# Kernel optimization log

Hardware: AMD Instinct MI355X
Metric: run time of the kernel (lower is better)

## Reference

```python
import jax, jax.numpy as jnp
import numpy as np

B, S, D = 2, 2048, 1024
H, DK, DV = 16, 64, 64
DFF = 4096
EPS_RMS = 1e-6


def setup_inputs() -> dict:
    key = jax.random.key(0)
    ks = jax.random.split(key, 10)
    sc = 0.02
    return {
        "x": jax.random.normal(ks[0], (B, S, D), jnp.float32),
        "w_q": jax.random.normal(ks[1], (D, H * DK), jnp.float32) * sc,
        "w_k": jax.random.normal(ks[2], (D, H * DK), jnp.float32) * sc,
        "w_v": jax.random.normal(ks[3], (D, H * DV), jnp.float32) * sc,
        "w_o": jax.random.normal(ks[4], (H * DV, D), jnp.float32) * sc,
        "w_gate": jax.random.normal(ks[5], (D, DFF), jnp.float32) * sc,
        "w_up": jax.random.normal(ks[6], (D, DFF), jnp.float32) * sc,
        "w_down": jax.random.normal(ks[7], (DFF, D), jnp.float32) * sc,
        "g1": jnp.ones((D,), jnp.float32),
        "g2": jnp.ones((D,), jnp.float32),
    }


def _rmsnorm(x, g):
    var = jnp.mean(jnp.square(x), axis=-1, keepdims=True)
    return x * jax.lax.rsqrt(var + EPS_RMS) * g


def _stable_softmax(s):
    # Faithful to source: exp(x) / (sum exp(x) + 1e-9); fully-masked rows -> 0.
    e = jnp.exp(s)
    return e / (jnp.sum(e, axis=-1, keepdims=True) + 1e-9)


def reference(x, w_q, w_k, w_v, w_o, w_gate, w_up, w_down, g1, g2):
    b, s, d = x.shape
    h = _rmsnorm(x, g1)
    q = (h @ w_q).reshape(b, s, H, DK).transpose(0, 2, 1, 3)  # [B,H,S,DK]
    k = (h @ w_k).reshape(b, s, H, DK).transpose(0, 2, 1, 3)
    v = (h @ w_v).reshape(b, s, H, DV).transpose(0, 2, 1, 3)
    scores = jnp.einsum("bhqd,bhkd->bhqk", q, k) / jnp.sqrt(jnp.asarray(DK, x.dtype))
    # triu with diagonal=0: self and future positions are masked
    mask = jnp.triu(jnp.ones((s, s), bool))
    scores = jnp.where(mask, -jnp.inf, scores)
    attn = _stable_softmax(scores)  # [B,H,S,S]
    av = jnp.einsum("bhqk,bhkd->bhqd", attn, v)
    av = av.transpose(0, 2, 1, 3).reshape(b, s, H * DV)
    x = x + av @ w_o  # residual 1
    h2 = _rmsnorm(x, g2)
    hidden = jax.nn.silu(h2 @ w_gate) * (h2 @ w_up)
    return x + hidden @ w_down  # residual 2
```

## Files before the change

kernel.cpp:

```cpp
#include <hip/hip_runtime.h>
#include <cstdint>
#include <cstddef>

typedef unsigned short u16;
typedef unsigned char u8;
typedef unsigned int u32;
typedef __bf16 bf16x8 __attribute__((ext_vector_type(8)));
typedef float floatx4 __attribute__((ext_vector_type(4)));
typedef float floatx16 __attribute__((ext_vector_type(16)));
typedef int i32x8 __attribute__((ext_vector_type(8)));

#define B_ 2
#define S_ 2048
#define D_ 1024
#define H_ 16
#define DFF_ 4096
#define BS_ 4096

__device__ __forceinline__ u16 f2bf(float f) {
  u32 u = __builtin_bit_cast(u32, f);
  u += 0x7fffu + ((u >> 16) & 1u);
  return (u16)(u >> 16);
}
__device__ __forceinline__ float bf2f(u16 h) {
  u32 u = ((u32)h) << 16;
  return __builtin_bit_cast(float, u);
}

__device__ __forceinline__ u32 cvtpk_bf16(float lo, float hi) {
  u32 r;
  asm("v_cvt_pk_bf16_f32 %0, %1, %2" : "=v"(r) : "v"(lo), "v"(hi));
  return r;
}

__device__ __forceinline__ float fexp2(float x) {
  float r;
  asm("v_exp_f32 %0, %1" : "=v"(r) : "v"(x));
  return r;
}

__device__ __forceinline__ u32 f2e4m3(float f) {
  u32 u = __builtin_bit_cast(u32, f);
  const u32 s = (u >> 24) & 0x80u;
  const u32 au = u & 0x7fffffffu;
  if (au < 0x3c800000u) return s;
  if (au > 0x43e00000u) return s | 0x7eu;
  const u32 lsb = (au >> 20) & 1u;
  const u32 r = au + 0x0007ffffu + lsb;
  const u32 e = (r >> 23) & 0xffu;
  const u32 m = (r >> 20) & 7u;
  return s | (((e - 120u) & 0xfu) << 3) | m;
}

__device__ __forceinline__ void gl_lds16(const void* g, void* l) {
  __builtin_amdgcn_global_load_lds(
      (const __attribute__((address_space(1))) void*)g,
      (__attribute__((address_space(3))) void*)l, 16, 0, 0);
}

__device__ __forceinline__ void xcd_swz(int GX, int GY, int& bx, int& by) {
  int flat = by * GX + bx;
  const int q = (GX * GY) >> 3;
  flat = (flat & 7) * q + (flat >> 3);
  bx = flat % GX;
  by = flat / GX;
}

#define WAITB(N) asm volatile("s_waitcnt vmcnt(" #N ")\n\ts_barrier" ::: "memory")

__global__ void prep_weights(const float* __restrict__ wq, const float* __restrict__ wk,
                             const float* __restrict__ wv, const float* __restrict__ wo,
                             const float* __restrict__ wg, const float* __restrict__ wu,
                             const float* __restrict__ wd,
                             u16* __restrict__ wqkv_t, u16* __restrict__ wo_t,
                             u8* __restrict__ wguf8, u16* __restrict__ wdn_t) {
  __shared__ float tile[32][33];
  const int id = blockIdx.x;
  const float* src;
  u16* dst = nullptr;
  int R, C, bx, by, mode;
  if (id < 3072) {
    const int which = id >> 10, lo = id & 1023;
    src = which == 0 ? wq : (which == 1 ? wk : wv);
    dst = wqkv_t + which * 1024 * 1024;
    R = 1024; C = 1024; bx = lo & 31; by = lo >> 5; mode = 0;
  } else if (id < 4096) {
    const int lo = id - 3072;
    src = wo; dst = wo_t; R = 1024; C = 1024; bx = lo & 31; by = lo >> 5; mode = 0;
  } else if (id < 8192) {
    const int lo = id - 4096;
    src = wg; R = 1024; C = 4096; bx = lo & 127; by = lo >> 7; mode = 1;
  } else if (id < 12288) {
    const int lo = id - 8192;
    src = wu; R = 1024; C = 4096; bx = lo & 127; by = lo >> 7; mode = 2;
  } else {
    const int lo = id - 12288;
    src = wd; dst = wdn_t; R = 4096; C = 1024; bx = lo & 31; by = lo >> 5; mode = 0;
  }
  const int tx = threadIdx.x, ty = threadIdx.y;
  const int c0 = bx * 32, r0 = by * 32;
#pragma unroll
  for (int i = 0; i < 4; i++)
    tile[ty + i * 8][tx] = src[(size_t)(r0 + ty + i * 8) * C + c0 + tx];
  __syncthreads();
  const int sx = ty * 32 + tx;
  const int oci = sx >> 3, cg = (sx & 7) * 4;
  const int oc = c0 + oci;
  const float v0 = tile[cg][oci], v1 = tile[cg + 1][oci];
  const float v2 = tile[cg + 2][oci], v3 = tile[cg + 3][oci];
  if (mode == 0) {
    uint2 o;
    o.x = (u32)f2bf(v0) | ((u32)f2bf(v1) << 16);
    o.y = (u32)f2bf(v2) | ((u32)f2bf(v3) << 16);
    *(uint2*)(dst + (size_t)oc * R + r0 + cg) = o;
  } else {
    const int orow = (oc >> 5) * 64 + (oc & 31) + (mode == 2 ? 32 : 0);
    const u32 p = f2e4m3(v0 * 64.f) | (f2e4m3(v1 * 64.f) << 8) |
                  (f2e4m3(v2 * 64.f) << 16) | (f2e4m3(v3 * 64.f) << 24);
    *(u32*)(wguf8 + (size_t)orow * 1024 + r0 + cg) = p;
  }
}

template <int F8>
__global__ __launch_bounds__(256) void rmsnorm_kernel(const float* __restrict__ x,
                                                      const float* __restrict__ g,
                                                      void* __restrict__ out) {
  const int row = blockIdx.x, t = threadIdx.x;
  const float4 v = ((const float4*)(x + (size_t)row * 1024))[t];
  float ss = v.x * v.x + v.y * v.y + v.z * v.z + v.w * v.w;
#pragma unroll
  for (int off = 32; off > 0; off >>= 1) ss += __shfl_xor(ss, off);
  __shared__ float red[4];
  if ((t & 63) == 0) red[t >> 6] = ss;
  __syncthreads();
  ss = red[0] + red[1] + red[2] + red[3];
  const float inv = rsqrtf(ss * (1.0f / 1024.0f) + 1e-6f);
  const float4 gv = ((const float4*)g)[t];
  const float y0 = v.x * inv * gv.x, y1 = v.y * inv * gv.y;
  const float y2 = v.z * inv * gv.z, y3 = v.w * inv * gv.w;
  if (F8) {
    const u32 p = f2e4m3(y0) | (f2e4m3(y1) << 8) | (f2e4m3(y2) << 16) | (f2e4m3(y3) << 24);
    ((u32*)out)[(size_t)row * 256 + t] = p;
  } else {
    uint2 o;
    o.x = (u32)f2bf(y0) | ((u32)f2bf(y1) << 16);
    o.y = (u32)f2bf(y2) | ((u32)f2bf(y3) << 16);
    ((uint2*)out)[(size_t)row * 256 + t] = o;
  }
}

template <int BN>
__device__ __forceinline__ void bt_step(const u16* Asb, const u16* Bsb,
                                        floatx16 (&acc)[2][BN / 64],
                                        int wm, int wn, int c31, int khalf) {
  constexpr int NTI = BN / 64;
#pragma unroll
  for (int ks = 0; ks < 4; ks++) {
    bf16x8 af[2], bfr[NTI];
#pragma unroll
    for (int mi = 0; mi < 2; mi++) {
      const int row = wm * 64 + mi * 32 + c31;
      const int e = (ks * 2 + khalf) ^ (row & 7);
      af[mi] = *(const bf16x8*)(Asb + row * 64 + e * 8);
    }
#pragma unroll
    for (int ni = 0; ni < NTI; ni++) {
      const int row = wn * (BN / 2) + ni * 32 + c31;
      const int e = (ks * 2 + khalf) ^ (row & 7);
      bfr[ni] = *(const bf16x8*)(Bsb + row * 64 + e * 8);
    }
    __builtin_amdgcn_s_setprio(1);
#pragma unroll
    for (int mi = 0; mi < 2; mi++)
#pragma unroll
      for (int ni = 0; ni < NTI; ni++)
        acc[mi][ni] = __builtin_amdgcn_mfma_f32_32x32x16_bf16(af[mi], bfr[ni],
                                                              acc[mi][ni], 0, 0, 0);
    __builtin_amdgcn_s_setprio(0);
  }
}

template <int SPW>
__device__ __forceinline__ void bt_issue(const u16* (&gsrc)[SPW], u16* const (&ld0)[SPW],
                                         int bufofs) {
#pragma unroll
  for (int i = 0; i < SPW; i++) gl_lds16(gsrc[i], ld0[i] + bufofs);
#pragma unroll
  for (int i = 0; i < SPW; i++) gsrc[i] += 64;
}

template <int BN, int EPI>
__global__ __launch_bounds__(256) void gemm_bt(const u16* __restrict__ A,
                                               const u16* __restrict__ Bt,
                                               void* __restrict__ Cout,
                                               const float* __restrict__ res,
                                               u16* __restrict__ vTout,
                                               int M, int N, int K) {
  constexpr int NTI = BN / 64;
  constexpr int ASZ = 128 * 64;
  constexpr int BSZ = BN * 64;
  constexpr int STRIDE = ASZ + BSZ;
  __shared__ u16 SMEM[3 * STRIDE];
  constexpr int NSEG = 16 + BN / 8;
  constexpr int SPW = NSEG / 4;
  static_assert(SPW == 6, "vmcnt literal assumes 6 loads/wave/tile");
  const int t = threadIdx.x, w = t >> 6, l = t & 63;

  int bx = (int)blockIdx.x, by = (int)blockIdx.y;
  xcd_swz((int)gridDim.x, (int)gridDim.y, bx, by);
  const int m0 = by * 128, n0 = bx * BN;
  const int wm = w >> 1, wn = w & 1;
  const int c31 = l & 31, khalf = l >> 5;

  const u16* gsrc[SPW];
  u16* ld0[SPW];
  {
    const int rl = l >> 3, ch = (l & 7) ^ rl;
#pragma unroll
    for (int i = 0; i < SPW; i++) {
      const int s = w * SPW + i;
      if (s < 16) {
        gsrc[i] = A + (size_t)(m0 + s * 8 + rl) * K + ch * 8;
        ld0[i] = SMEM + s * 512;
      } else {
        gsrc[i] = Bt + (size_t)(n0 + (s - 16) * 8 + rl) * K + ch * 8;
        ld0[i] = SMEM + ASZ + (s - 16) * 512;
      }
    }
  }

  floatx16 acc[2][NTI] = {};

#define BT_STEP(CB) bt_step<BN>(SMEM + (CB)*STRIDE, SMEM + (CB)*STRIDE + ASZ, \
                                acc, wm, wn, c31, khalf)

  bt_issue<SPW>(gsrc, ld0, 0 * STRIDE);
  bt_issue<SPW>(gsrc, ld0, 1 * STRIDE);
  const int NT = K >> 6;
  for (int rep = 0; rep < (NT - 4) / 3; rep++) {
    WAITB(6); bt_issue<SPW>(gsrc, ld0, 2 * STRIDE); BT_STEP(0);
    WAITB(6); bt_issue<SPW>(gsrc, ld0, 0 * STRIDE); BT_STEP(1);
    WAITB(6); bt_issue<SPW>(gsrc, ld0, 1 * STRIDE); BT_STEP(2);
  }
  WAITB(6); bt_issue<SPW>(gsrc, ld0, 2 * STRIDE); BT_STEP(0);
  WAITB(6); bt_issue<SPW>(gsrc, ld0, 0 * STRIDE); BT_STEP(1);
  WAITB(6); BT_STEP(2);
  WAITB(0); BT_STEP(0);
#undef BT_STEP

  if constexpr (EPI == 3) {
    if (n0 >= 2048) {
#pragma unroll
      for (int mi = 0; mi < 2; mi++)
#pragma unroll
        for (int ni = 0; ni < NTI; ni++) {
          const int col = n0 + wn * (BN / 2) + ni * 32 + c31 - 2048;
          const int hh = col >> 6, dv = col & 63;
          const int rbase = m0 + wm * 64 + mi * 32 + 4 * khalf;
          const int bb = rbase >> 11;
          u16* vp = vTout + (size_t)((bb * 16 + hh) * 64 + dv) * 2048 + (rbase & 2047);
#pragma unroll
          for (int rg = 0; rg < 4; rg++) {
            uint2 pk;
            pk.x = (u32)f2bf(acc[mi][ni][rg * 4 + 0]) |
                   ((u32)f2bf(acc[mi][ni][rg * 4 + 1]) << 16);
            pk.y = (u32)f2bf(acc[mi][ni][rg * 4 + 2]) |
                   ((u32)f2bf(acc[mi][ni][rg * 4 + 3]) << 16);
            *(uint2*)(vp + rg * 8) = pk;
          }
        }
      return;
    }
  }
#pragma unroll
  for (int mi = 0; mi < 2; mi++)
#pragma unroll
    for (int ni = 0; ni < NTI; ni++) {
      const int col = n0 + wn * (BN / 2) + ni * 32 + c31;
#pragma unroll
      for (int reg = 0; reg < 16; reg++) {
        const int row = m0 + wm * 64 + mi * 32 + (reg & 3) + 8 * (reg >> 2) + 4 * khalf;
        const size_t idx = (size_t)row * N + col;
        if (EPI == 1) ((float*)Cout)[idx] = acc[mi][ni][reg] + res[idx];
        else          ((u16*)Cout)[idx] = f2bf(acc[mi][ni][reg]);
      }
    }
}

__device__ __forceinline__ void f8_step(const u8* Asb, const u8* Bsb,
                                        floatx16 (&acc)[2][2],
                                        int wm, int wn, int c31, int hf) {
  i32x8 af[2], bf[2];
#pragma unroll
  for (int mi = 0; mi < 2; mi++) {
    const int r = wm * 64 + mi * 32 + c31;
    const int g = (r >> 1) & 3;
    const uint4 lo = *(const uint4*)(Asb + r * 64 + ((2 * hf) ^ g) * 16);
    const uint4 hi = *(const uint4*)(Asb + r * 64 + ((2 * hf + 1) ^ g) * 16);
    af[mi] = i32x8{(int)lo.x, (int)lo.y, (int)lo.z, (int)lo.w,
                   (int)hi.x, (int)hi.y, (int)hi.z, (int)hi.w};
  }
#pragma unroll
  for (int ni = 0; ni < 2; ni++) {
    const int r = wn * 64 + ni * 32 + c31;
    const int g = (r >> 1) & 3;
    const uint4 lo = *(const uint4*)(Bsb + r * 64 + ((2 * hf) ^ g) * 16);
    const uint4 hi = *(const uint4*)(Bsb + r * 64 + ((2 * hf + 1) ^ g) * 16);
    bf[ni] = i32x8{(int)lo.x, (int)lo.y, (int)lo.z, (int)lo.w,
                   (int)hi.x, (int)hi.y, (int)hi.z, (int)hi.w};
  }
  __builtin_amdgcn_s_setprio(1);
#pragma unroll
  for (int mi = 0; mi < 2; mi++)
#pragma unroll
    for (int ni = 0; ni < 2; ni++)
      acc[mi][ni] = __builtin_amdgcn_mfma_scale_f32_32x32x64_f8f6f4(
          af[mi], bf[ni], acc[mi][ni], 0, 0,
          0, 0x7F7F7F7F,
          0, 0x79797979);
  __builtin_amdgcn_s_setprio(0);
}

__device__ __forceinline__ void f8_issue(const u8* (&gsrc)[4], u8* const (&ld0)[4],
                                         int bufofs) {
#pragma unroll
  for (int i = 0; i < 4; i++) gl_lds16(gsrc[i], ld0[i] + bufofs);
#pragma unroll
  for (int i = 0; i < 4; i++) gsrc[i] += 64;
}

__global__ __launch_bounds__(256) void gemm_f8(const u8* __restrict__ A,
                                               const u8* __restrict__ B,
                                               u16* __restrict__ hid,
                                               int M, int K) {
  constexpr int STRIDE = 2 * 128 * 64;
  __shared__ u8 SMEM[3 * STRIDE];
  const int t = threadIdx.x, w = t >> 6, l = t & 63;
  int bx = (int)blockIdx.x, by = (int)blockIdx.y;
  xcd_swz((int)gridDim.x, (int)gridDim.y, bx, by);
  const int m0 = by * 128, n0 = bx * 128;
  const int wm = w >> 1, wn = w & 1;
  const int c31 = l & 31, hf = l >> 5;

  const u8* gsrc[4];
  u8* ld0[4];
  {
    const int rl = l >> 2, ch = (l & 3) ^ ((l >> 3) & 3);
#pragma unroll
    for (int i = 0; i < 4; i++) {
      const int s = w * 4 + i;
      if (s < 8) {
        gsrc[i] = A + (size_t)(m0 + s * 16 + rl) * K + ch * 16;
        ld0[i] = SMEM + s * 1024;
      } else {
        gsrc[i] = B + (size_t)(n0 + (s - 8) * 16 + rl) * K + ch * 16;
        ld0[i] = SMEM + 8192 + (s - 8) * 1024;
      }
    }
  }

  floatx16 acc[2][2] = {};

#define F8_STEP(CB) f8_step(SMEM + (CB)*STRIDE, SMEM + (CB)*STRIDE + 8192, \
                            acc, wm, wn, c31, hf)

  f8_issue(gsrc, ld0, 0 * STRIDE);
  f8_issue(gsrc, ld0, 1 * STRIDE);
  const int NT = K >> 6;
  for (int rep = 0; rep < (NT - 4) / 3; rep++) {
    WAITB(4); f8_issue(gsrc, ld0, 2 * STRIDE); F8_STEP(0);
    WAITB(4); f8_issue(gsrc, ld0, 0 * STRIDE); F8_STEP(1);
    WAITB(4); f8_issue(gsrc, ld0, 1 * STRIDE); F8_STEP(2);
  }
  WAITB(4); f8_issue(gsrc, ld0, 2 * STRIDE); F8_STEP(0);
  WAITB(4); f8_issue(gsrc, ld0, 0 * STRIDE); F8_STEP(1);
  WAITB(4); F8_STEP(2);
  WAITB(0); F8_STEP(0);
#undef F8_STEP

#pragma unroll
  for (int mi = 0; mi < 2; mi++) {
    const int colo = (bx * 2 + wn) * 32 + c31;
#pragma unroll
    for (int reg = 0; reg < 16; reg++) {
      const int row = m0 + wm * 64 + mi * 32 + (reg & 3) + 8 * (reg >> 2) + 4 * hf;
      const float g = acc[mi][0][reg];
      const float u = acc[mi][1][reg];
      hid[(size_t)row * 4096 + colo] = f2bf(g / (1.f + __expf(-g)) * u);
    }
  }
}

__global__ __launch_bounds__(256) void attn_kernel(const u16* __restrict__ qkv,
                                                   const u16* __restrict__ vT,
                                                   u16* __restrict__ av) {
  __shared__ u16 SM[2 * 8192];
  __shared__ u16 Ps[4 * 2048];
  const int t = threadIdx.x, w = t >> 6, l = t & 63;
  const int lrow = l & 15, lk = l >> 4;
  const int bh = blockIdx.x;
  const int b = bh >> 4, h = bh & 15;
  const int qt = 15 - (int)blockIdx.y;
  const int qbase = qt * 128 + w * 32;
  const int ktmax = 2 * qt + 1;
  u16* Pw = Ps + w * 2048;
  const float SC = 0.125f * 1.44269504088896f;

  bf16x8 aq[2][2];
#pragma unroll
  for (int sub = 0; sub < 2; sub++)
#pragma unroll
    for (int half = 0; half < 2; half++)
      aq[sub][half] = *(const bf16x8*)(qkv + (size_t)(b * S_ + qbase + sub * 16 + lrow) * 3072 +
                                       h * 64 + half * 32 + lk * 8);

  const u16* gcur[4];
  int gstep[4], loff[4];
#pragma unroll
  for (int i = 0; i < 4; i++) {
    const int c = w + 4 * i;
    const int half = (c >> 2) & 1, grp = c & 3;
    if (c < 8) {
      gcur[i] = qkv + (size_t)(b * S_ + grp * 16 + (l >> 2)) * 3072 + D_ + h * 64 +
                half * 32 + (l & 3) * 8;
      gstep[i] = 64 * 3072;
      loff[i] = half * 2048 + grp * 512;
    } else {
      gcur[i] = vT + (size_t)(bh * 64 + grp * 16 + (l >> 2)) * S_ + half * 32 + (l & 3) * 8;
      gstep[i] = 64;
      loff[i] = 4096 + half * 2048 + grp * 512;
    }
  }

  floatx4 oacc[2][4] = {};
  float den[2] = {0.f, 0.f};

  int cur = 0;
#pragma unroll
  for (int i = 0; i < 4; i++) { gl_lds16(gcur[i], SM + loff[i]); gcur[i] += gstep[i]; }

  for (int kt = 0; kt <= ktmax; kt++) {
    __syncthreads();
    if (kt < ktmax) {
#pragma unroll
      for (int i = 0; i < 4; i++) {
        gl_lds16(gcur[i], SM + (cur ^ 1) * 8192 + loff[i]);
        gcur[i] += gstep[i];
      }
    }
    const u16* Kbuf = SM + cur * 8192;
    const u16* Vbuf = Kbuf + 4096;

    const bool active = (kt * 64 < qbase + 31);
    if (active) {
      const bool need_mask = (kt * 64 + 64 > qbase);

      bf16x8 bk[4][2];
#pragma unroll
      for (int ct = 0; ct < 4; ct++)
#pragma unroll
        for (int half = 0; half < 2; half++)
          bk[ct][half] = *(const bf16x8*)(Kbuf + half * 2048 + (ct * 16 + lrow) * 32 + lk * 8);

      floatx4 sf[2][4] = {};
      __builtin_amdgcn_s_setprio(1);
#pragma unroll
      for (int sub = 0; sub < 2; sub++)
#pragma unroll
        for (int ct = 0; ct < 4; ct++) {
          sf[sub][ct] = __builtin_amdgcn_mfma_f32_16x16x32_bf16(bk[ct][0], aq[sub][0],
                                                                sf[sub][ct], 0, 0, 0);
          sf[sub][ct] = __builtin_amdgcn_mfma_f32_16x16x32_bf16(bk[ct][1], aq[sub][1],
                                                                sf[sub][ct], 0, 0, 0);
        }
      __builtin_amdgcn_s_setprio(0);

      if (!need_mask) {
#pragma unroll
        for (int sub = 0; sub < 2; sub++) {
          const int prow = sub * 16 + lrow;
#pragma unroll
          for (int ct = 0; ct < 4; ct++) {
            const float p0 = fexp2(sf[sub][ct][0] * SC);
            const float p1 = fexp2(sf[sub][ct][1] * SC);
            const float p2 = fexp2(sf[sub][ct][2] * SC);
            const float p3 = fexp2(sf[sub][ct][3] * SC);
            den[sub] += (p0 + p1) + (p2 + p3);
            uint2 pk;
            pk.x = cvtpk_bf16(p0, p1);
            pk.y = cvtpk_bf16(p2, p3);
            *(uint2*)(Pw + prow * 64 + (((2 * ct + (lk >> 1)) ^ (lrow & 7)) << 3) +
                      (lk & 1) * 4) = pk;
          }
        }
      } else {
#pragma unroll
        for (int sub = 0; sub < 2; sub++) {
          const int qp = qbase + sub * 16 + lrow;
          const int prow = sub * 16 + lrow;
#pragma unroll
          for (int ct = 0; ct < 4; ct++) {
            const int kb = kt * 64 + ct * 16 + lk * 4;
            const float p0 = (kb + 0 < qp) ? fexp2(sf[sub][ct][0] * SC) : 0.f;
            const float p1 = (kb + 1 < qp) ? fexp2(sf[sub][ct][1] * SC) : 0.f;
            const float p2 = (kb + 2 < qp) ? fexp2(sf[sub][ct][2] * SC) : 0.f;
            const float p3 = (kb + 3 < qp) ? fexp2(sf[sub][ct][3] * SC) : 0.f;
            den[sub] += (p0 + p1) + (p2 + p3);
            uint2 pk;
            pk.x = cvtpk_bf16(p0, p1);
            pk.y = cvtpk_bf16(p2, p3);
            *(uint2*)(Pw + prow * 64 + (((2 * ct + (lk >> 1)) ^ (lrow & 7)) << 3) +
                      (lk & 1) * 4) = pk;
          }
        }
      }

      bf16x8 ap[2][2], bv[4][2];
#pragma unroll
      for (int sub = 0; sub < 2; sub++)
#pragma unroll
        for (int kh = 0; kh < 2; kh++) {
          const int prow = sub * 16 + lrow;
          ap[sub][kh] = *(const bf16x8*)(Pw + prow * 64 + (((kh * 4 + lk) ^ (prow & 7)) << 3));
        }
#pragma unroll
      for (int ni = 0; ni < 4; ni++)
#pragma unroll
        for (int kh = 0; kh < 2; kh++)
          bv[ni][kh] = *(const bf16x8*)(Vbuf + kh * 2048 + (ni * 16 + lrow) * 32 + lk * 8);
      __builtin_amdgcn_s_setprio(1);
#pragma unroll
      for (int sub = 0; sub < 2; sub++)
#pragma unroll
        for (int ni = 0; ni < 4; ni++) {
          oacc[sub][ni] = __builtin_amdgcn_mfma_f32_16x16x32_bf16(ap[sub][0], bv[ni][0],
                                                                  oacc[sub][ni], 0, 0, 0);
          oacc[sub][ni] = __builtin_amdgcn_mfma_f32_16x16x32_bf16(ap[sub][1], bv[ni][1],
                                                                  oacc[sub][ni], 0, 0, 0);
        }
      __builtin_amdgcn_s_setprio(0);
    }
    cur ^= 1;
  }

#pragma unroll
  for (int sub = 0; sub < 2; sub++) {
    den[sub] += __shfl_xor(den[sub], 16);
    den[sub] += __shfl_xor(den[sub], 32);
  }
  float dq[2][4];
#pragma unroll
  for (int sub = 0; sub < 2; sub++)
#pragma unroll
    for (int r = 0; r < 4; r++)
      dq[sub][r] = __shfl(den[sub], lk * 4 + r);

#pragma unroll
  for (int sub = 0; sub < 2; sub++)
#pragma unroll
    for (int ni = 0; ni < 4; ni++)
#pragma unroll
      for (int r = 0; r < 4; r++) {
        const int row = qbase + sub * 16 + lk * 4 + r;
        const int col = h * 64 + ni * 16 + lrow;
        av[(size_t)(b * S_ + row) * 1024 + col] = f2bf(oacc[sub][ni][r] / (dq[sub][r] + 1e-9f));
      }
}

#define OFF_WQKV 0u
#define OFF_WO   6291456u
#define OFF_WGU8 8388608u
#define OFF_WDN  16777216u
#define OFF_H1   25165824u
#define OFF_QKV  33554432u
#define OFF_VT   58720256u
#define OFF_AV   67108864u
#define OFF_X1   75497472u
#define OFF_H2F8 92274688u
#define OFF_HID  96468992u

extern "C" void kernel_launch(void* const* d_in, const int* in_sizes, int n_in,
                              void* d_out, int out_size, void* d_ws, size_t ws_size,
                              hipStream_t stream) {
  const float* x      = (const float*)d_in[0];
  const float* w_q    = (const float*)d_in[1];
  const float* w_k    = (const float*)d_in[2];
  const float* w_v    = (const float*)d_in[3];
  const float* w_o    = (const float*)d_in[4];
  const float* w_gate = (const float*)d_in[5];
  const float* w_up   = (const float*)d_in[6];
  const float* w_down = (const float*)d_in[7];
  const float* g1     = (const float*)d_in[8];
  const float* g2     = (const float*)d_in[9];

  char* ws = (char*)d_ws;
  u16* wqkv_t = (u16*)(ws + OFF_WQKV);
  u16* wo_t   = (u16*)(ws + OFF_WO);
  u8*  wguf8  = (u8*)(ws + OFF_WGU8);
  u16* wdn_t  = (u16*)(ws + OFF_WDN);
  u16* h1     = (u16*)(ws + OFF_H1);
  u16* qkv    = (u16*)(ws + OFF_QKV);
  u16* vT     = (u16*)(ws + OFF_VT);
  u16* av     = (u16*)(ws + OFF_AV);
  float* x1   = (float*)(ws + OFF_X1);
  u8*  h2f8   = (u8*)(ws + OFF_H2F8);
  u16* hid    = (u16*)(ws + OFF_HID);
  float* out  = (float*)d_out;

  prep_weights<<<16384, dim3(32, 8), 0, stream>>>(w_q, w_k, w_v, w_o, w_gate, w_up, w_down,
                                                  wqkv_t, wo_t, wguf8, wdn_t);

  rmsnorm_kernel<0><<<BS_, 256, 0, stream>>>(x, g1, h1);
  gemm_bt<64, 3><<<dim3(3072 / 64, BS_ / 128), 256, 0, stream>>>(
      h1, wqkv_t, qkv, nullptr, vT, BS_, 3072, 1024);
  attn_kernel<<<dim3(32, 16), 256, 0, stream>>>(qkv, vT, av);
  gemm_bt<64, 1><<<dim3(1024 / 64, BS_ / 128), 256, 0, stream>>>(
      av, wo_t, x1, x, nullptr, BS_, 1024, 1024);
  rmsnorm_kernel<1><<<BS_, 256, 0, stream>>>(x1, g2, h2f8);
  gemm_f8<<<dim3(4096 / 64, BS_ / 128), 256, 0, stream>>>(h2f8, wguf8, hid, BS_, 1024);
  gemm_bt<64, 1><<<dim3(1024 / 64, BS_ / 128), 256, 0, stream>>>(
      hid, wdn_t, out, x1, nullptr, BS_, 1024, 4096);
}
```

Baseline: 348.2 us.

## Enlarge QKV and gate/up GEMM tiles with a double-buffered pipeline for BN=128

Raises the QKV projection GEMM to 128-wide N tiles, using a new double-buffered, barrier-synchronised pipeline for that tile size. Doubles the FP8 gate/up GEMM N tile to 256, so each wave computes four MFMA column tiles and the SiLU epilogue handles two gate/up pairs. Removes the s_setprio hints around the MFMA blocks. The aim is more reuse of operands loaded into LDS and fewer blocks, at the cost of more registers and LDS per block and possibly lower occupancy.

```diff
diff --git a/kernel.cpp b/kernel.cpp
--- a/kernel.cpp
+++ b/kernel.cpp
@@ -169,14 +169,12 @@
       const int e = (ks * 2 + khalf) ^ (row & 7);
       bfr[ni] = *(const bf16x8*)(Bsb + row * 64 + e * 8);
     }
-    __builtin_amdgcn_s_setprio(1);
 #pragma unroll
     for (int mi = 0; mi < 2; mi++)
 #pragma unroll
       for (int ni = 0; ni < NTI; ni++)
         acc[mi][ni] = __builtin_amdgcn_mfma_f32_32x32x16_bf16(af[mi], bfr[ni],
                                                               acc[mi][ni], 0, 0, 0);
-    __builtin_amdgcn_s_setprio(0);
   }
 }
 
@@ -198,12 +196,11 @@
                                                int M, int N, int K) {
   constexpr int NTI = BN / 64;
   constexpr int ASZ = 128 * 64;
-  constexpr int BSZ = BN * 64;
-  constexpr int STRIDE = ASZ + BSZ;
-  __shared__ u16 SMEM[3 * STRIDE];
+  constexpr int STRIDE = ASZ + BN * 64;
+  constexpr int NBUF = (BN == 64) ? 3 : 2;
+  __shared__ u16 SMEM[NBUF * STRIDE];
   constexpr int NSEG = 16 + BN / 8;
   constexpr int SPW = NSEG / 4;
-  static_assert(SPW == 6, "vmcnt literal assumes 6 loads/wave/tile");
   const int t = threadIdx.x, w = t >> 6, l = t & 63;
 
   int bx = (int)blockIdx.x, by = (int)blockIdx.y;
@@ -234,18 +231,34 @@
 #define BT_STEP(CB) bt_step<BN>(SMEM + (CB)*STRIDE, SMEM + (CB)*STRIDE + ASZ, \
                                 acc, wm, wn, c31, khalf)
 
-  bt_issue<SPW>(gsrc, ld0, 0 * STRIDE);
-  bt_issue<SPW>(gsrc, ld0, 1 * STRIDE);
-  const int NT = K >> 6;
-  for (int rep = 0; rep < (NT - 4) / 3; rep++) {
+  if constexpr (BN == 64) {
+    bt_issue<SPW>(gsrc, ld0, 0 * STRIDE);
+    bt_issue<SPW>(gsrc, ld0, 1 * STRIDE);
+    const int NT = K >> 6;
+    for (int rep = 0; rep < (NT - 4) / 3; rep++) {
+      WAITB(6); bt_issue<SPW>(gsrc, ld0, 2 * STRIDE); BT_STEP(0);
+      WAITB(6); bt_issue<SPW>(gsrc, ld0, 0 * STRIDE); BT_STEP(1);
+      WAITB(6); bt_issue<SPW>(gsrc, ld0, 1 * STRIDE); BT_STEP(2);
+    }
     WAITB(6); bt_issue<SPW>(gsrc, ld0, 2 * STRIDE); BT_STEP(0);
     WAITB(6); bt_issue<SPW>(gsrc, ld0, 0 * STRIDE); BT_STEP(1);
-    WAITB(6); bt_issue<SPW>(gsrc, ld0, 1 * STRIDE); BT_STEP(2);
-  }
-  WAITB(6); bt_issue<SPW>(gsrc, ld0, 2 * STRIDE); BT_STEP(0);
-  WAITB(6); bt_issue<SPW>(gsrc, ld0, 0 * STRIDE); BT_STEP(1);
-  WAITB(6); BT_STEP(2);
-  WAITB(0); BT_STEP(0);
+    WAITB(6); BT_STEP(2);
+    WAITB(0); BT_STEP(0);
+  } else {
+    bt_issue<SPW>(gsrc, ld0, 0 * STRIDE);
+    bt_issue<SPW>(gsrc, ld0, 1 * STRIDE);
+    const int NT = K >> 6;
+    for (int kk = 0; kk < NT - 2; kk += 2) {
+      WAITB(8); BT_STEP(0);
+      __builtin_amdgcn_s_barrier();
+      bt_issue<SPW>(gsrc, ld0, 0 * STRIDE);
+      WAITB(8); BT_STEP(1);
+      __builtin_amdgcn_s_barrier();
+      bt_issue<SPW>(gsrc, ld0, 1 * STRIDE);
+    }
+    WAITB(8); BT_STEP(0);
+    WAITB(0); BT_STEP(1);
+  }
 #undef BT_STEP
 
   if constexpr (EPI == 3) {
@@ -288,9 +301,9 @@
 }
 
 __device__ __forceinline__ void f8_step(const u8* Asb, const u8* Bsb,
-                                        floatx16 (&acc)[2][2],
+                                        floatx16 (&acc)[2][4],
                                         int wm, int wn, int c31, int hf) {
-  i32x8 af[2], bf[2];
+  i32x8 af[2], bf[4];
 #pragma unroll
   for (int mi = 0; mi < 2; mi++) {
     const int r = wm * 64 + mi * 32 + c31;
@@ -301,54 +314,52 @@
                    (int)hi.x, (int)hi.y, (int)hi.z, (int)hi.w};
   }
 #pragma unroll
-  for (int ni = 0; ni < 2; ni++) {
-    const int r = wn * 64 + ni * 32 + c31;
+  for (int ni = 0; ni < 4; ni++) {
+    const int r = wn * 128 + ni * 32 + c31;
     const int g = (r >> 1) & 3;
     const uint4 lo = *(const uint4*)(Bsb + r * 64 + ((2 * hf) ^ g) * 16);
     const uint4 hi = *(const uint4*)(Bsb + r * 64 + ((2 * hf + 1) ^ g) * 16);
     bf[ni] = i32x8{(int)lo.x, (int)lo.y, (int)lo.z, (int)lo.w,
                    (int)hi.x, (int)hi.y, (int)hi.z, (int)hi.w};
   }
-  __builtin_amdgcn_s_setprio(1);
 #pragma unroll
   for (int mi = 0; mi < 2; mi++)
 #pragma unroll
-    for (int ni = 0; ni < 2; ni++)
+    for (int ni = 0; ni < 4; ni++)
       acc[mi][ni] = __builtin_amdgcn_mfma_scale_f32_32x32x64_f8f6f4(
           af[mi], bf[ni], acc[mi][ni], 0, 0,
           0, 0x7F7F7F7F,
           0, 0x79797979);
-  __builtin_amdgcn_s_setprio(0);
-}
-
-__device__ __forceinline__ void f8_issue(const u8* (&gsrc)[4], u8* const (&ld0)[4],
+}
+
+__device__ __forceinline__ void f8_issue(const u8* (&gsrc)[6], u8* const (&ld0)[6],
                                          int bufofs) {
 #pragma unroll
-  for (int i = 0; i < 4; i++) gl_lds16(gsrc[i], ld0[i] + bufofs);
-#pragma unroll
-  for (int i = 0; i < 4; i++) gsrc[i] += 64;
+  for (int i = 0; i < 6; i++) gl_lds16(gsrc[i], ld0[i] + bufofs);
+#pragma unroll
+  for (int i = 0; i < 6; i++) gsrc[i] += 64;
 }
 
 __global__ __launch_bounds__(256) void gemm_f8(const u8* __restrict__ A,
                                                const u8* __restrict__ B,
                                                u16* __restrict__ hid,
                                                int M, int K) {
-  constexpr int STRIDE = 2 * 128 * 64;
+  constexpr int STRIDE = (128 + 256) * 64;
   __shared__ u8 SMEM[3 * STRIDE];
   const int t = threadIdx.x, w = t >> 6, l = t & 63;
   int bx = (int)blockIdx.x, by = (int)blockIdx.y;
   xcd_swz((int)gridDim.x, (int)gridDim.y, bx, by);
-  const int m0 = by * 128, n0 = bx * 128;
+  const int m0 = by * 128, n0 = bx * 256;
   const int wm = w >> 1, wn = w & 1;
   const int c31 = l & 31, hf = l >> 5;
 
-  const u8* gsrc[4];
-  u8* ld0[4];
+  const u8* gsrc[6];
+  u8* ld0[6];
   {
     const int rl = l >> 2, ch = (l & 3) ^ ((l >> 3) & 3);
 #pragma unroll
-    for (int i = 0; i < 4; i++) {
-      const int s = w * 4 + i;
+    for (int i = 0; i < 6; i++) {
+      const int s = w * 6 + i;
       if (s < 8) {
         gsrc[i] = A + (size_t)(m0 + s * 16 + rl) * K + ch * 16;
         ld0[i] = SMEM + s * 1024;
@@ -359,7 +370,7 @@
     }
   }
 
-  floatx16 acc[2][2] = {};
+  floatx16 acc[2][4] = {};
 
 #define F8_STEP(CB) f8_step(SMEM + (CB)*STRIDE, SMEM + (CB)*STRIDE + 8192, \
                             acc, wm, wn, c31, hf)
@@ -368,27 +379,29 @@
   f8_issue(gsrc, ld0, 1 * STRIDE);
   const int NT = K >> 6;
   for (int rep = 0; rep < (NT - 4) / 3; rep++) {
-    WAITB(4); f8_issue(gsrc, ld0, 2 * STRIDE); F8_STEP(0);
-    WAITB(4); f8_issue(gsrc, ld0, 0 * STRIDE); F8_STEP(1);
-    WAITB(4); f8_issue(gsrc, ld0, 1 * STRIDE); F8_STEP(2);
-  }
-  WAITB(4); f8_issue(gsrc, ld0, 2 * STRIDE); F8_STEP(0);
-  WAITB(4); f8_issue(gsrc, ld0, 0 * STRIDE); F8_STEP(1);
-  WAITB(4); F8_STEP(2);
+    WAITB(6); f8_issue(gsrc, ld0, 2 * STRIDE); F8_STEP(0);
+    WAITB(6); f8_issue(gsrc, ld0, 0 * STRIDE); F8_STEP(1);
+    WAITB(6); f8_issue(gsrc, ld0, 1 * STRIDE); F8_STEP(2);
+  }
+  WAITB(6); f8_issue(gsrc, ld0, 2 * STRIDE); F8_STEP(0);
+  WAITB(6); f8_issue(gsrc, ld0, 0 * STRIDE); F8_STEP(1);
+  WAITB(6); F8_STEP(2);
   WAITB(0); F8_STEP(0);
 #undef F8_STEP
 
 #pragma unroll
-  for (int mi = 0; mi < 2; mi++) {
-    const int colo = (bx * 2 + wn) * 32 + c31;
-#pragma unroll
-    for (int reg = 0; reg < 16; reg++) {
-      const int row = m0 + wm * 64 + mi * 32 + (reg & 3) + 8 * (reg >> 2) + 4 * hf;
-      const float g = acc[mi][0][reg];
-      const float u = acc[mi][1][reg];
-      hid[(size_t)row * 4096 + colo] = f2bf(g / (1.f + __expf(-g)) * u);
-    }
-  }
+  for (int mi = 0; mi < 2; mi++)
+#pragma unroll
+    for (int j = 0; j < 2; j++) {
+      const int colo = (bx * 4 + wn * 2 + j) * 32 + c31;
+#pragma unroll
+      for (int reg = 0; reg < 16; reg++) {
+        const int row = m0 + wm * 64 + mi * 32 + (reg & 3) + 8 * (reg >> 2) + 4 * hf;
+        const float g = acc[mi][2 * j][reg];
+        const float u = acc[mi][2 * j + 1][reg];
+        hid[(size_t)row * 4096 + colo] = f2bf(g / (1.f + __expf(-g)) * u);
+      }
+    }
 }
 
 __global__ __launch_bounds__(256) void attn_kernel(const u16* __restrict__ qkv,
@@ -611,13 +624,13 @@
                                                   wqkv_t, wo_t, wguf8, wdn_t);
 
   rmsnorm_kernel<0><<<BS_, 256, 0, stream>>>(x, g1, h1);
-  gemm_bt<64, 3><<<dim3(3072 / 64, BS_ / 128), 256, 0, stream>>>(
+  gemm_bt<128, 3><<<dim3(3072 / 128, BS_ / 128), 256, 0, stream>>>(
       h1, wqkv_t, qkv, nullptr, vT, BS_, 3072, 1024);
   attn_kernel<<<dim3(32, 16), 256, 0, stream>>>(qkv, vT, av);
   gemm_bt<64, 1><<<dim3(1024 / 64, BS_ / 128), 256, 0, stream>>>(
       av, wo_t, x1, x, nullptr, BS_, 1024, 1024);
   rmsnorm_kernel<1><<<BS_, 256, 0, stream>>>(x1, g2, h2f8);
-  gemm_f8<<<dim3(4096 / 64, BS_ / 128), 256, 0, stream>>>(h2f8, wguf8, hid, BS_, 1024);
+  gemm_f8<<<dim3(8192 / 256, BS_ / 128), 256, 0, stream>>>(h2f8, wguf8, hid, BS_, 1024);
   gemm_bt<64, 1><<<dim3(1024 / 64, BS_ / 128), 256, 0, stream>>>(
       hid, wdn_t, out, x1, nullptr, BS_, 1024, 4096);
 }
```

Measured after the change: 339.1 us. 1.03x faster.
